# Optimization experiments

Measured on AMD Instinct MI355X. Metric: run time of the kernel, lower is better.

## Reference

```python
import jax, jax.numpy as jnp
import numpy as np

HEADS = 16
DIM_HEAD = 64
SCALE = DIM_HEAD ** -0.5


def setup_inputs() -> dict:
    key = jax.random.key(0)
    k1, k2, k3 = jax.random.split(key, 3)
    B, C, N = 2, 1024, 2048
    h_dim = HEADS * DIM_HEAD  # 1024
    x = jax.random.normal(k1, (B, C, N), dtype=jnp.float32)
    w_qkv = jax.random.normal(k2, (3 * h_dim, C), dtype=jnp.float32) * (C ** -0.5)
    w_out = jax.random.normal(k3, (C, h_dim), dtype=jnp.float32) * (h_dim ** -0.5)
    b_out = jnp.zeros((C,), dtype=jnp.float32)
    return {"x": x, "w_qkv": w_qkv, "w_out": w_out, "b_out": b_out}


def reference(x, w_qkv, w_out, b_out):
    B, C, N = x.shape
    h_dim = HEADS * DIM_HEAD
    # 1x1 conv == pointwise matmul over channel dim: [3h_dim, C] x [B, C, N]
    qkv = jnp.einsum('oc,bcn->bon', w_qkv, x)
    q, k, v = jnp.split(qkv, 3, axis=1)  # each [B, h_dim, N]
    def heads(t):
        return t.reshape(B, HEADS, DIM_HEAD, N)  # b h d n
    q, k, v = heads(q), heads(k), heads(v)
    sim = jnp.einsum('bhdi,bhdj->bhij', q * SCALE, k)  # [B, H, N, N]
    attn = jax.nn.softmax(sim, axis=-1)  # stable softmax (max-subtract fused)
    out = jnp.einsum('bhij,bhdj->bhid', attn, v)  # [B, H, N, D]
    out = out.transpose(0, 1, 3, 2).reshape(B, h_dim, N)  # b (h d) n
    out = jnp.einsum('oc,bcn->bon', w_out, out) + b_out[None, :, None]
    return out
```

## Files before the change

### kernel.cpp

```cpp
#include <hip/hip_runtime.h>
#include <hip/hip_bf16.h>

#define BATCH 2
#define CIN   1024
#define NN    2048
#define HEADS 16
#define DHEAD 64
#define HDIM  1024
#define O3    3072
#define QSCALE 0.125f
#define QSCALE_L2E 0.18033688011112042f
#define QSZ ((size_t)BATCH * HEADS * NN * DHEAD)

typedef unsigned short ushort_t;
typedef __attribute__((ext_vector_type(8))) short bf16x8;
typedef __attribute__((ext_vector_type(8))) unsigned short ushort8;
typedef __attribute__((ext_vector_type(4))) unsigned short ushort4v;
typedef __attribute__((ext_vector_type(16))) float f32x16;

__device__ inline ushort_t f2bf(float f) {
    unsigned u = __builtin_bit_cast(unsigned, f);
    unsigned r = u + 0x7fffu + ((u >> 16) & 1u);
    return (ushort_t)(r >> 16);
}
__device__ inline float bf2f(ushort_t h) {
    return __builtin_bit_cast(float, (unsigned)h << 16);
}
__device__ inline f32x16 mfma32(bf16x8 a, bf16x8 b, f32x16 c) {
    return __builtin_amdgcn_mfma_f32_32x32x16_bf16(a, b, c, 0, 0, 0);
}
__device__ inline unsigned cvt_pk_bf16(float a, float b) {
    unsigned r;
    asm("v_cvt_pk_bf16_f32 %0, %1, %2" : "=v"(r) : "v"(a), "v"(b));
    return r;
}

union U4 { unsigned u[4]; bf16x8 v; };

#define GLDS(gp, lp) __builtin_amdgcn_global_load_lds( \
    (__attribute__((address_space(1))) void*)(gp),     \
    (__attribute__((address_space(3))) void*)(lp), 16, 0, 0)

__global__ __launch_bounds__(256) void convert_two(const float* __restrict__ in1,
                                                   ushort_t* __restrict__ out1,
                                                   int n8_1,
                                                   const float* __restrict__ in2,
                                                   ushort_t* __restrict__ out2,
                                                   int n8_2) {
    int t = blockIdx.x * 256 + threadIdx.x;
    const float* in = in1;
    ushort_t* out = out1;
    if (t >= n8_1) {
        t -= n8_1;
        if (t >= n8_2) return;
        in = in2;
        out = out2;
    }
    size_t base = (size_t)t * 8;
    float4 a = *(const float4*)(in + base);
    float4 b = *(const float4*)(in + base + 4);
    float v[8] = {a.x, a.y, a.z, a.w, b.x, b.y, b.z, b.w};
    ushort8 hv;
#pragma unroll
    for (int i = 0; i < 8; ++i) hv[i] = f2bf(v[i]);
    *(ushort8*)(out + base) = hv;
}

__global__ __launch_bounds__(256) void transpose_cvt(const float* __restrict__ in,
                                                     ushort_t* __restrict__ th) {
    __shared__ float T[32][33];
    const int b = blockIdx.z;
    const int n0 = blockIdx.x * 32, c0 = blockIdx.y * 32;
    const int t = threadIdx.x;
    const int r = t >> 3, q = t & 7;
    float4 v = *(const float4*)(in + ((size_t)b * CIN + c0 + r) * NN + n0 + q * 4);
    T[r][q * 4 + 0] = v.x; T[r][q * 4 + 1] = v.y;
    T[r][q * 4 + 2] = v.z; T[r][q * 4 + 3] = v.w;
    __syncthreads();
    ushort4v hv;
#pragma unroll
    for (int i = 0; i < 4; ++i) hv[i] = f2bf(T[q * 4 + i][r]);
    size_t o = ((size_t)b * NN + n0 + r) * CIN + c0 + q * 4;
    *(ushort4v*)(th + o) = hv;
}

template<int MODE>
__global__ __launch_bounds__(256, 3) void gemm_mfma(
    const ushort_t* __restrict__ Ah, const ushort_t* __restrict__ Bth,
    const float* __restrict__ bias, float* __restrict__ outF,
    ushort_t* __restrict__ Qh, ushort_t* __restrict__ Kf,
    ushort_t* __restrict__ Vf) {

    __shared__ __align__(16) ushort_t lsAh[4096], lsBh[4096];

    const int b  = blockIdx.z;
    const int n0 = blockIdx.x * 128;
    const int m0 = blockIdx.y * 128;
    const int tid = threadIdx.x;
    const int wave = tid >> 6, lane = tid & 63;
    const int l31 = lane & 31, hi5 = lane >> 5;
    const int wr = wave >> 1, wc = wave & 1;

    const int srow = lane >> 2;
    const int kswz = 8 * ((lane & 3) ^ ((lane >> 3) & 3));
    const ushort_t* gAh = Ah  + (size_t)(m0 + wave * 16 + srow) * CIN + kswz;
    const ushort_t* gBh = Bth + ((size_t)b * NN + n0 + wave * 16 + srow) * CIN + kswz;
    ushort_t* dAh = lsAh + wave * 512;
    ushort_t* dBh = lsBh + wave * 512;

    const int rswz = ((l31 >> 1) & 3) * 8;
    int offA[2][2], offB[2][2];
#pragma unroll
    for (int f = 0; f < 2; ++f)
#pragma unroll
        for (int kh = 0; kh < 2; ++kh) {
            offA[f][kh] = (wr * 64 + f * 32 + l31) * 64 + ((kh * 16 + hi5 * 8) ^ rswz) * 2;
            offB[f][kh] = (wc * 64 + f * 32 + l31) * 64 + ((kh * 16 + hi5 * 8) ^ rswz) * 2;
        }

    f32x16 acc[2][2];
#pragma unroll
    for (int i = 0; i < 2; ++i)
#pragma unroll
        for (int j = 0; j < 2; ++j)
#pragma unroll
            for (int r = 0; r < 16; ++r) acc[i][j][r] = 0.f;

    for (int k0 = 0; k0 < CIN; k0 += 32) {
        __syncthreads();
        GLDS(gAh + k0,            dAh);
        GLDS(gAh + 64 * CIN + k0, dAh + 2048);
        GLDS(gBh + k0,            dBh);
        GLDS(gBh + 64 * CIN + k0, dBh + 2048);
        __syncthreads();
#pragma unroll
        for (int kh = 0; kh < 2; ++kh) {
            bf16x8 a_h[2], b_h[2];
#pragma unroll
            for (int f = 0; f < 2; ++f) {
                a_h[f] = *(const bf16x8*)((const char*)lsAh + offA[f][kh]);
                b_h[f] = *(const bf16x8*)((const char*)lsBh + offB[f][kh]);
            }
#pragma unroll
            for (int fi = 0; fi < 2; ++fi)
#pragma unroll
                for (int fj = 0; fj < 2; ++fj)
                    acc[fi][fj] = mfma32(a_h[fi], b_h[fj], acc[fi][fj]);
        }
    }

    const int nn = n0 + wc * 64 + l31;

    if constexpr (MODE == 0) {
        const int region = m0 >> 10;
        if (region == 0) {
            const int head = ((m0 & 1023) >> 6) + wr;
            const size_t bh_base = (size_t)(b * HEADS + head) * NN;
#pragma unroll
            for (int fj = 0; fj < 2; ++fj) {
                const size_t rowb = (bh_base + nn + fj * 32) * DHEAD;
#pragma unroll
                for (int fi = 0; fi < 2; ++fi)
#pragma unroll
                    for (int g = 0; g < 4; ++g) {
                        ushort4v hv;
#pragma unroll
                        for (int i = 0; i < 4; ++i)
                            hv[i] = f2bf(acc[fi][fj][4 * g + i] * QSCALE_L2E);
                        *(ushort4v*)(Qh + rowb + fi * 32 + 4 * hi5 + 8 * g) = hv;
                    }
            }
        } else if (region == 1) {
            const int head = ((m0 & 1023) >> 6) + wr;
            const size_t bhk = (size_t)(b * HEADS + head);
#pragma unroll
            for (int fj = 0; fj < 2; ++fj) {
                const int j = nn + fj * 32;
                const size_t jbb = (bhk * 64 + (j >> 5)) * 4;
#pragma unroll
                for (int fi = 0; fi < 2; ++fi)
#pragma unroll
                    for (int g = 0; g < 4; ++g) {
                        ushort4v hv;
#pragma unroll
                        for (int i = 0; i < 4; ++i)
                            hv[i] = f2bf(acc[fi][fj][4 * g + i]);
                        const int c = fi * 2 + (g >> 1);
                        const int lk = (g & 1) * 32 + l31;
                        *(ushort4v*)(Kf + ((jbb + c) * 64 + lk) * 8 + 4 * hi5) = hv;
                    }
            }
        } else {
            const int ch0 = (m0 - 2048) + wr * 64;
#pragma unroll
            for (int fi = 0; fi < 2; ++fi)
#pragma unroll
                for (int fj = 0; fj < 2; ++fj) {
                    const int j = nn + fj * 32;
                    const int jb = j >> 5, kh2 = (j >> 4) & 1;
                    const int lvh = ((j >> 3) & 1) * 32;
                    const int e = j & 7;
#pragma unroll
                    for (int r = 0; r < 16; ++r) {
                        const int ch = ch0 + fi * 32 + (r & 3) + 8 * (r >> 2) + 4 * hi5;
                        const int head = ch >> 6, d = ch & 63;
                        const size_t idx =
                            (((((size_t)(b * HEADS + head) * 64 + jb) * 2 + kh2) * 2 +
                              (d >> 5)) * 64 + lvh + (d & 31)) * 8 + e;
                        Vf[idx] = f2bf(acc[fi][fj][r]);
                    }
                }
        }
    } else {
#pragma unroll
        for (int fi = 0; fi < 2; ++fi)
#pragma unroll
            for (int fj = 0; fj < 2; ++fj)
#pragma unroll
                for (int r = 0; r < 16; ++r) {
                    const int mrow = m0 + wr * 64 + fi * 32 + (r & 3) + 8 * (r >> 2) + 4 * hi5;
                    outF[((size_t)b * CIN + mrow) * NN + nn + fj * 32] =
                        acc[fi][fj][r] + bias[mrow];
                }
    }
}

__global__ __launch_bounds__(512, 3) void attn_mfma(
    const ushort_t* __restrict__ Qh, const ushort_t* __restrict__ Kf,
    const ushort_t* __restrict__ Vf,
    ushort_t* __restrict__ aoth) {
    const int Lid = blockIdx.x;
    const int slot = Lid & 7, rest = Lid >> 3;
    const int bh = slot * 4 + (rest >> 4);
    const int qt = rest & 15;
    const int b = bh >> 4, h = bh & 15;
    const int w = threadIdx.x >> 6;
    const int team = w >> 2;
    const int tw = w & 3;
    const int lane = threadIdx.x & 63;
    const int l31 = lane & 31;
    const int hi5 = lane >> 5;
    const int q0 = qt * 128 + tw * 32;

    __shared__ float oS[128 * 65];
    __shared__ float lS[128];

    bf16x8 qfh[4];
    {
        const ushort_t* qb = Qh + ((size_t)bh * NN + q0 + l31) * DHEAD + hi5 * 8;
#pragma unroll
        for (int c = 0; c < 4; ++c) qfh[c] = *(const bf16x8*)(qb + c * 16);
    }

    const ushort_t* kp0 = Kf + ((size_t)bh * 64 + team * 32) * 2048 + lane * 8;
    const ushort_t* vp0 = Vf + ((size_t)bh * 64 + team * 32) * 2048 + lane * 8;

    f32x16 o0, o1, zz;
#pragma unroll
    for (int r = 0; r < 16; ++r) { o0[r] = 0.f; o1[r] = 0.f; zz[r] = 0.f; }
    float l = 0.f;

#define ATTN_LOAD(P, JB)                                                       \
    {                                                                          \
        const ushort_t* kq_ = kp0 + (size_t)(JB) * 2048;                       \
        const ushort_t* vq_ = vp0 + (size_t)(JB) * 2048;                       \
        P##k0 = *(const bf16x8*)(kq_);                                         \
        P##k1 = *(const bf16x8*)(kq_ + 512);                                   \
        P##k2 = *(const bf16x8*)(kq_ + 1024);                                  \
        P##k3 = *(const bf16x8*)(kq_ + 1536);                                  \
        P##v0 = *(const bf16x8*)(vq_);                                         \
        P##v1 = *(const bf16x8*)(vq_ + 512);                                   \
        P##v2 = *(const bf16x8*)(vq_ + 1024);                                  \
        P##v3 = *(const bf16x8*)(vq_ + 1536);                                  \
    }

#define ATTN_STEP(K0, K1, K2, K3, V0, V1, V2, V3)                              \
    {                                                                          \
        __builtin_amdgcn_s_setprio(1);                                         \
        f32x16 sS = mfma32(K0, qfh[0], zz);                                    \
        sS = mfma32(K1, qfh[1], sS);                                           \
        sS = mfma32(K2, qfh[2], sS);                                           \
        sS = mfma32(K3, qfh[3], sS);                                           \
        __builtin_amdgcn_s_setprio(0);                                         \
        f32x16 s;                                                              \
        _Pragma("unroll") for (int r = 0; r < 16; ++r)                         \
            s[r] = __builtin_amdgcn_exp2f(sS[r]);                              \
        float t0 = (s[0] + s[1]) + (s[2] + s[3]);                              \
        float t1 = (s[4] + s[5]) + (s[6] + s[7]);                              \
        float t2 = (s[8] + s[9]) + (s[10] + s[11]);                            \
        float t3 = (s[12] + s[13]) + (s[14] + s[15]);                          \
        l += (t0 + t1) + (t2 + t3);                                            \
        unsigned Q0 = cvt_pk_bf16(s[0], s[1]);                                 \
        unsigned Q1 = cvt_pk_bf16(s[2], s[3]);                                 \
        unsigned Q2 = cvt_pk_bf16(s[4], s[5]);                                 \
        unsigned Q3 = cvt_pk_bf16(s[6], s[7]);                                 \
        asm("v_permlane32_swap_b32 %0, %1" : "+v"(Q0), "+v"(Q2));              \
        asm("v_permlane32_swap_b32 %0, %1" : "+v"(Q1), "+v"(Q3));              \
        unsigned R0 = cvt_pk_bf16(s[8], s[9]);                                 \
        unsigned R1 = cvt_pk_bf16(s[10], s[11]);                               \
        unsigned R2 = cvt_pk_bf16(s[12], s[13]);                               \
        unsigned R3 = cvt_pk_bf16(s[14], s[15]);                               \
        asm("v_permlane32_swap_b32 %0, %1" : "+v"(R0), "+v"(R2));              \
        asm("v_permlane32_swap_b32 %0, %1" : "+v"(R1), "+v"(R3));              \
        U4 thA; thA.u[0] = Q0; thA.u[1] = Q1; thA.u[2] = Q2; thA.u[3] = Q3;    \
        U4 thB; thB.u[0] = R0; thB.u[1] = R1; thB.u[2] = R2; thB.u[3] = R3;    \
        bf16x8 pB0 = thA.v, pB1 = thB.v;                                       \
        __builtin_amdgcn_s_setprio(1);                                         \
        o0 = mfma32(V0, pB0, o0);                                              \
        o1 = mfma32(V1, pB0, o1);                                              \
        o0 = mfma32(V2, pB1, o0);                                              \
        o1 = mfma32(V3, pB1, o1);                                              \
        __builtin_amdgcn_s_setprio(0);                                         \
    }

    bf16x8 ak0, ak1, ak2, ak3, av0, av1, av2, av3;
    bf16x8 bk0, bk1, bk2, bk3, bv0, bv1, bv2, bv3;
    ATTN_LOAD(a, 0);
#pragma unroll 1
    for (int jb = 0; jb < 32; jb += 2) {
        ATTN_LOAD(b, jb + 1);
        ATTN_STEP(ak0, ak1, ak2, ak3, av0, av1, av2, av3);
        ATTN_LOAD(a, (jb + 2) & 31);
        ATTN_STEP(bk0, bk1, bk2, bk3, bv0, bv1, bv2, bv3);
    }
#undef ATTN_LOAD
#undef ATTN_STEP

    l += __shfl_xor(l, 32);
    const int q = tw * 32 + l31;
    if (team == 1) {
#pragma unroll
        for (int dt = 0; dt < 2; ++dt)
#pragma unroll
            for (int r = 0; r < 16; ++r) {
                const int d = dt * 32 + (r & 3) + 8 * (r >> 2) + 4 * hi5;
                oS[q * 65 + d] = dt ? o1[r] : o0[r];
            }
        if (hi5 == 0) lS[q] = l;
    }
    __syncthreads();
    if (team == 0) {
        const float invl = 1.0f / (l + lS[q]);
        const size_t rowb = ((size_t)b * NN + q0 + l31) * HDIM + h * DHEAD;
#pragma unroll
        for (int dt = 0; dt < 2; ++dt)
#pragma unroll
            for (int g = 0; g < 4; ++g) {
                ushort4v hv;
#pragma unroll
                for (int i = 0; i < 4; ++i) {
                    const int r = 4 * g + i;
                    const int d = dt * 32 + i + 8 * g + 4 * hi5;
                    float f = ((dt ? o1[r] : o0[r]) + oS[q * 65 + d]) * invl;
                    hv[i] = f2bf(f);
                }
                size_t o = rowb + dt * 32 + 8 * g + 4 * hi5;
                *(ushort4v*)(aoth + o) = hv;
            }
    }
}

extern "C" void kernel_launch(void* const* d_in, const int* in_sizes, int n_in,
                              void* d_out, int out_size, void* d_ws, size_t ws_size,
                              hipStream_t stream) {
    const float* x     = (const float*)d_in[0];
    const float* w_qkv = (const float*)d_in[1];
    const float* w_out = (const float*)d_in[2];
    const float* b_out = (const float*)d_in[3];
    float* out = (float*)d_out;

    ushort_t* ws_u = (ushort_t*)d_ws;
    ushort_t* Qh = ws_u;
    ushort_t* Kf = Qh + QSZ;
    ushort_t* Vf = Kf + QSZ;
    ushort_t* woh = ws_u + 3 * QSZ;
    ushort_t* shared_u = ws_u + 6 * QSZ;
    ushort_t* wqh = shared_u;
    ushort_t* aoth = shared_u;
    ushort_t* xth = (ushort_t*)d_out;

    if (ws_size < (6 * QSZ + 2 * (size_t)BATCH * NN * CIN) * sizeof(ushort_t)) return;

    convert_two<<<2048, 256, 0, stream>>>(w_qkv, wqh, O3 * CIN / 8,
                                          w_out, woh, CIN * HDIM / 8);
    transpose_cvt<<<dim3(NN / 32, CIN / 32, BATCH), 256, 0, stream>>>(x, xth);

    gemm_mfma<0><<<dim3(NN / 128, O3 / 128, BATCH), 256, 0, stream>>>(
        wqh, xth, nullptr, nullptr, Qh, Kf, Vf);

    attn_mfma<<<dim3(512), 512, 0, stream>>>(Qh, Kf, Vf, aoth);

    gemm_mfma<1><<<dim3(NN / 128, HDIM / 128, BATCH), 256, 0, stream>>>(
        woh, aoth, b_out, out, nullptr, nullptr, nullptr);
}
```

Before: 117.8 us.

## Process two query tiles per wave to reuse K/V fragments in attention

Halves the attention block to 256 threads, and each wave now handles two 32-row query tiles that share the same K and V register fragments. The goal is to halve global K/V load traffic per query and give the MFMA units more independent work between loads. In exchange, register pressure roughly doubles for accumulators and Q fragments, and fewer waves remain to hide latency.

```diff
diff --git a/kernel.cpp b/kernel.cpp
--- a/kernel.cpp
+++ b/kernel.cpp
@@ -225,7 +225,7 @@
     }
 }
 
-__global__ __launch_bounds__(512, 3) void attn_mfma(
+__global__ __launch_bounds__(256, 2) void attn_mfma(
     const ushort_t* __restrict__ Qh, const ushort_t* __restrict__ Kf,
     const ushort_t* __restrict__ Vf,
     ushort_t* __restrict__ aoth) {
@@ -235,30 +235,37 @@
     const int qt = rest & 15;
     const int b = bh >> 4, h = bh & 15;
     const int w = threadIdx.x >> 6;
-    const int team = w >> 2;
-    const int tw = w & 3;
+    const int team = w >> 1;
+    const int qp = w & 1;
     const int lane = threadIdx.x & 63;
     const int l31 = lane & 31;
     const int hi5 = lane >> 5;
-    const int q0 = qt * 128 + tw * 32;
+    const int q0a = qt * 128 + qp * 64;
+    const int q0b = q0a + 32;
 
     __shared__ float oS[128 * 65];
     __shared__ float lS[128];
 
-    bf16x8 qfh[4];
+    bf16x8 qfa[4], qfb[4];
     {
-        const ushort_t* qb = Qh + ((size_t)bh * NN + q0 + l31) * DHEAD + hi5 * 8;
-#pragma unroll
-        for (int c = 0; c < 4; ++c) qfh[c] = *(const bf16x8*)(qb + c * 16);
+        const ushort_t* qa = Qh + ((size_t)bh * NN + q0a + l31) * DHEAD + hi5 * 8;
+        const ushort_t* qb = Qh + ((size_t)bh * NN + q0b + l31) * DHEAD + hi5 * 8;
+#pragma unroll
+        for (int c = 0; c < 4; ++c) {
+            qfa[c] = *(const bf16x8*)(qa + c * 16);
+            qfb[c] = *(const bf16x8*)(qb + c * 16);
+        }
     }
 
     const ushort_t* kp0 = Kf + ((size_t)bh * 64 + team * 32) * 2048 + lane * 8;
     const ushort_t* vp0 = Vf + ((size_t)bh * 64 + team * 32) * 2048 + lane * 8;
 
-    f32x16 o0, o1, zz;
-#pragma unroll
-    for (int r = 0; r < 16; ++r) { o0[r] = 0.f; o1[r] = 0.f; zz[r] = 0.f; }
-    float l = 0.f;
+    f32x16 o0a, o1a, o0b, o1b, zz;
+#pragma unroll
+    for (int r = 0; r < 16; ++r) {
+        o0a[r] = 0.f; o1a[r] = 0.f; o0b[r] = 0.f; o1b[r] = 0.f; zz[r] = 0.f;
+    }
+    float la = 0.f, lb = 0.f;
 
 #define ATTN_LOAD(P, JB)                                                       \
     {                                                                          \
@@ -274,22 +281,16 @@
         P##v3 = *(const bf16x8*)(vq_ + 1536);                                  \
     }
 
-#define ATTN_STEP(K0, K1, K2, K3, V0, V1, V2, V3)                              \
+#define ATTN_CHAIN(SS, QF, V0, V1, V2, V3, O0, O1, LACC)                       \
     {                                                                          \
-        __builtin_amdgcn_s_setprio(1);                                         \
-        f32x16 sS = mfma32(K0, qfh[0], zz);                                    \
-        sS = mfma32(K1, qfh[1], sS);                                           \
-        sS = mfma32(K2, qfh[2], sS);                                           \
-        sS = mfma32(K3, qfh[3], sS);                                           \
-        __builtin_amdgcn_s_setprio(0);                                         \
         f32x16 s;                                                              \
         _Pragma("unroll") for (int r = 0; r < 16; ++r)                         \
-            s[r] = __builtin_amdgcn_exp2f(sS[r]);                              \
+            s[r] = __builtin_amdgcn_exp2f(SS[r]);                              \
         float t0 = (s[0] + s[1]) + (s[2] + s[3]);                              \
         float t1 = (s[4] + s[5]) + (s[6] + s[7]);                              \
         float t2 = (s[8] + s[9]) + (s[10] + s[11]);                            \
         float t3 = (s[12] + s[13]) + (s[14] + s[15]);                          \
-        l += (t0 + t1) + (t2 + t3);                                            \
+        LACC += (t0 + t1) + (t2 + t3);                                         \
         unsigned Q0 = cvt_pk_bf16(s[0], s[1]);                                 \
         unsigned Q1 = cvt_pk_bf16(s[2], s[3]);                                 \
         unsigned Q2 = cvt_pk_bf16(s[4], s[5]);                                 \
@@ -306,11 +307,27 @@
         U4 thB; thB.u[0] = R0; thB.u[1] = R1; thB.u[2] = R2; thB.u[3] = R3;    \
         bf16x8 pB0 = thA.v, pB1 = thB.v;                                       \
         __builtin_amdgcn_s_setprio(1);                                         \
-        o0 = mfma32(V0, pB0, o0);                                              \
-        o1 = mfma32(V1, pB0, o1);                                              \
-        o0 = mfma32(V2, pB1, o0);                                              \
-        o1 = mfma32(V3, pB1, o1);                                              \
+        O0 = mfma32(V0, pB0, O0);                                              \
+        O1 = mfma32(V1, pB0, O1);                                              \
+        O0 = mfma32(V2, pB1, O0);                                              \
+        O1 = mfma32(V3, pB1, O1);                                              \
         __builtin_amdgcn_s_setprio(0);                                         \
+    }
+
+#define ATTN_STEP2(K0, K1, K2, K3, V0, V1, V2, V3)                             \
+    {                                                                          \
+        __builtin_amdgcn_s_setprio(1);                                         \
+        f32x16 sSa = mfma32(K0, qfa[0], zz);                                   \
+        sSa = mfma32(K1, qfa[1], sSa);                                         \
+        sSa = mfma32(K2, qfa[2], sSa);                                         \
+        sSa = mfma32(K3, qfa[3], sSa);                                         \
+        f32x16 sSb = mfma32(K0, qfb[0], zz);                                   \
+        sSb = mfma32(K1, qfb[1], sSb);                                         \
+        sSb = mfma32(K2, qfb[2], sSb);                                         \
+        sSb = mfma32(K3, qfb[3], sSb);                                         \
+        __builtin_amdgcn_s_setprio(0);                                         \
+        ATTN_CHAIN(sSa, qfa, V0, V1, V2, V3, o0a, o1a, la);                    \
+        ATTN_CHAIN(sSb, qfb, V0, V1, V2, V3, o0b, o1b, lb);                    \
     }
 
     bf16x8 ak0, ak1, ak2, ak3, av0, av1, av2, av3;
@@ -319,43 +336,52 @@
 #pragma unroll 1
     for (int jb = 0; jb < 32; jb += 2) {
         ATTN_LOAD(b, jb + 1);
-        ATTN_STEP(ak0, ak1, ak2, ak3, av0, av1, av2, av3);
+        ATTN_STEP2(ak0, ak1, ak2, ak3, av0, av1, av2, av3);
         ATTN_LOAD(a, (jb + 2) & 31);
-        ATTN_STEP(bk0, bk1, bk2, bk3, bv0, bv1, bv2, bv3);
+        ATTN_STEP2(bk0, bk1, bk2, bk3, bv0, bv1, bv2, bv3);
     }
 #undef ATTN_LOAD
-#undef ATTN_STEP
-
-    l += __shfl_xor(l, 32);
-    const int q = tw * 32 + l31;
+#undef ATTN_CHAIN
+#undef ATTN_STEP2
+
+    la += __shfl_xor(la, 32);
+    lb += __shfl_xor(lb, 32);
+    const int qA = qp * 64 + l31;
+    const int qB = qA + 32;
     if (team == 1) {
 #pragma unroll
         for (int dt = 0; dt < 2; ++dt)
 #pragma unroll
             for (int r = 0; r < 16; ++r) {
                 const int d = dt * 32 + (r & 3) + 8 * (r >> 2) + 4 * hi5;
-                oS[q * 65 + d] = dt ? o1[r] : o0[r];
+                oS[qA * 65 + d] = dt ? o1a[r] : o0a[r];
+                oS[qB * 65 + d] = dt ? o1b[r] : o0b[r];
             }
-        if (hi5 == 0) lS[q] = l;
+        if (hi5 == 0) { lS[qA] = la; lS[qB] = lb; }
     }
     __syncthreads();
     if (team == 0) {
-        const float invl = 1.0f / (l + lS[q]);
-        const size_t rowb = ((size_t)b * NN + q0 + l31) * HDIM + h * DHEAD;
+        const float invlA = 1.0f / (la + lS[qA]);
+        const float invlB = 1.0f / (lb + lS[qB]);
+        const size_t rowa = ((size_t)b * NN + q0a + l31) * HDIM + h * DHEAD;
+        const size_t rowbb = ((size_t)b * NN + q0b + l31) * HDIM + h * DHEAD;
 #pragma unroll
         for (int dt = 0; dt < 2; ++dt)
 #pragma unroll
             for (int g = 0; g < 4; ++g) {
-                ushort4v hv;
+                ushort4v hva, hvb;
 #pragma unroll
                 for (int i = 0; i < 4; ++i) {
                     const int r = 4 * g + i;
                     const int d = dt * 32 + i + 8 * g + 4 * hi5;
-                    float f = ((dt ? o1[r] : o0[r]) + oS[q * 65 + d]) * invl;
-                    hv[i] = f2bf(f);
+                    float fa = ((dt ? o1a[r] : o0a[r]) + oS[qA * 65 + d]) * invlA;
+                    float fb = ((dt ? o1b[r] : o0b[r]) + oS[qB * 65 + d]) * invlB;
+                    hva[i] = f2bf(fa);
+                    hvb[i] = f2bf(fb);
                 }
-                size_t o = rowb + dt * 32 + 8 * g + 4 * hi5;
-                *(ushort4v*)(aoth + o) = hv;
+                const size_t oo = dt * 32 + 8 * g + 4 * hi5;
+                *(ushort4v*)(aoth + rowa + oo) = hva;
+                *(ushort4v*)(aoth + rowbb + oo) = hvb;
             }
     }
 }
@@ -388,7 +414,7 @@
     gemm_mfma<0><<<dim3(NN / 128, O3 / 128, BATCH), 256, 0, stream>>>(
         wqh, xth, nullptr, nullptr, Qh, Kf, Vf);
 
-    attn_mfma<<<dim3(512), 512, 0, stream>>>(Qh, Kf, Vf, aoth);
+    attn_mfma<<<dim3(512), 256, 0, stream>>>(Qh, Kf, Vf, aoth);
 
     gemm_mfma<1><<<dim3(NN / 128, HDIM / 128, BATCH), 256, 0, stream>>>(
         woh, aoth, b_out, out, nullptr, nullptr, nullptr);
```

Result: faster. 113.8 us (-3.4%).
